# Performance work log

Measured on AMD Instinct MI355X. Metric: run time of the kernel, lower is better.

Reference implementation:

```python
import jax, jax.numpy as jnp
import numpy as np

B, T, D, H, OUT = 1024, 2048, 5, 64, 128


def _lstm_layer(x, Wih, Whh, bih, bhh):
    """PyTorch-convention LSTM layer. x: [B,T,Din]; gate order i,f,g,o."""
    b, t = x.shape[0], x.shape[1]
    h = Whh.shape[1]
    # Precompute input projections for all timesteps (the only big GEMM).
    xp = jnp.einsum('btd,gd->btg', x, Wih) + bih + bhh        # [B,T,4H]
    xp = jnp.swapaxes(xp, 0, 1)                               # [T,B,4H]

    def step(carry, xt):
        hprev, cprev = carry
        gates = xt + hprev @ Whh.T                            # [B,4H]
        i, f, g, o = jnp.split(gates, 4, axis=-1)
        i = jax.nn.sigmoid(i)
        f = jax.nn.sigmoid(f)
        g = jnp.tanh(g)
        o = jax.nn.sigmoid(o)
        c = f * cprev + i * g
        hnew = o * jnp.tanh(c)
        return (hnew, c), hnew

    h0 = jnp.zeros((b, h), x.dtype)
    (hT, cT), hs = jax.lax.scan(step, (h0, h0), xp)
    return jnp.swapaxes(hs, 0, 1), hT                         # [B,T,H], [B,H]


def setup_inputs() -> dict:
    key = jax.random.key(0)
    ks = jax.random.split(key, 11)
    s = 1.0 / np.sqrt(H)  # PyTorch LSTM init range

    def u(k, shape):
        return jax.random.uniform(k, shape, jnp.float32, -s, s)

    return {
        'x': jax.random.normal(ks[0], (B, T, D), jnp.float32),
        'W_ih0': u(ks[1], (4 * H, D)),
        'W_hh0': u(ks[2], (4 * H, H)),
        'b_ih0': u(ks[3], (4 * H,)),
        'b_hh0': u(ks[4], (4 * H,)),
        'W_ih1': u(ks[5], (4 * H, H)),
        'W_hh1': u(ks[6], (4 * H, H)),
        'b_ih1': u(ks[7], (4 * H,)),
        'b_hh1': u(ks[8], (4 * H,)),
        'W_fc': u(ks[9], (OUT, H)),
        'b_fc': u(ks[10], (OUT,)),
    }


def reference(x, W_ih0, W_hh0, b_ih0, b_hh0, W_ih1, W_hh1, b_ih1, b_hh1, W_fc, b_fc):
    # Layer 1 over raw 5-dim signal; inter-layer dropout is inactive at inference.
    y1, _ = _lstm_layer(x, W_ih0, W_hh0, b_ih0, b_hh0)
    # Layer 2; only its final hidden state hn[-1] is used downstream.
    _, h2 = _lstm_layer(y1, W_ih1, W_hh1, b_ih1, b_hh1)
    return jax.nn.relu(h2 @ W_fc.T + b_fc)                    # [B,128]
```

## Files before the change

### kernel.cpp

```cpp
#include <hip/hip_runtime.h>
#include <math.h>

#define BATCH 1024
#define TSEQ  2048
#define DIN   5
#define H     64
#define BT    4
#define SSTR  144
#define NOUT  128

typedef _Float16 f16x8 __attribute__((ext_vector_type(8)));
typedef float    f32x4 __attribute__((ext_vector_type(4)));

#if __has_builtin(__builtin_amdgcn_rcpf)
__device__ __forceinline__ float rcp_fast(float x) { return __builtin_amdgcn_rcpf(x); }
#else
__device__ __forceinline__ float rcp_fast(float x) { return 1.0f / x; }
#endif

#define LOG2E 1.44269504088896f
#define MFMA16(A, B, C) __builtin_amdgcn_mfma_f32_16x16x32_f16((A), (B), (C), 0, 0, 0)

__device__ __forceinline__ float sigm2(float s) {
    return rcp_fast(1.0f + __builtin_amdgcn_exp2f(-s));
}
__device__ __forceinline__ float tanh2(float s) {
    return fmaf(-2.0f, rcp_fast(__builtin_amdgcn_exp2f(s) + 1.0f), 1.0f);
}

__device__ __forceinline__ void sync_lgkm() {
    asm volatile("s_waitcnt lgkmcnt(0)" ::: "memory");
    __builtin_amdgcn_s_barrier();
    asm volatile("" ::: "memory");
}

__global__ __launch_bounds__(512)
void lstm_mfma(const float* __restrict__ x,
               const float* __restrict__ Wih0, const float* __restrict__ Whh0,
               const float* __restrict__ bih0, const float* __restrict__ bhh0,
               const float* __restrict__ Wih1, const float* __restrict__ Whh1,
               const float* __restrict__ bih1, const float* __restrict__ bhh1,
               const float* __restrict__ Wfc,  const float* __restrict__ bfc,
               float* __restrict__ out)
{
    __shared__ alignas(16) _Float16 S[2][BT * SSTR];
    __shared__ alignas(16) float    h2f[BT][H];

    const int tid  = threadIdx.x;
    const int w    = tid >> 6;
    const int lane = tid & 63;
    const int col  = lane & 15;
    const int q    = lane >> 4;
    const int ww   = w & 3;
    const int lay  = w >> 2;
    const int hu   = 16 * ww + col;
    const int b0   = blockIdx.x * BT;

    for (int j = tid; j < 2 * BT * SSTR; j += 512)
        ((_Float16*)S)[j] = (_Float16)0.0f;

    const float sgl[4] = {LOG2E, LOG2E, 2.0f * LOG2E, LOG2E};

    f16x8 Bf[4][4];
    f32x4 bC[4];
    float wx[4][DIN];
    float b1s[4];
    #pragma unroll
    for (int g = 0; g < 4; ++g) {
        const int   row = g * 64 + hu;
        const float sg  = sgl[g];
        if (lay) {
            const float* wa = Wih1 + row * H;
            const float* wb = Whh1 + row * H;
            #pragma unroll
            for (int j = 0; j < 8; ++j) {
                const int k = q * 8 + j;
                Bf[g][0][j] = (_Float16)(wa[k]      * sg);
                Bf[g][1][j] = (_Float16)(wa[32 + k] * sg);
                Bf[g][2][j] = (_Float16)(wb[k]      * sg);
                Bf[g][3][j] = (_Float16)(wb[32 + k] * sg);
            }
            const float bb = (bih1[row] + bhh1[row]) * sg;
            bC[g] = f32x4{bb, bb, bb, bb};
        } else {
            const float* wh = Whh0 + row * H;
            #pragma unroll
            for (int j = 0; j < 8; ++j) {
                const int k = q * 8 + j;
                Bf[g][0][j] = (_Float16)(wh[k]      * sg);
                Bf[g][1][j] = (_Float16)(wh[32 + k] * sg);
            }
            #pragma unroll
            for (int j = 0; j < DIN; ++j)
                wx[g][j] = Wih0[row * DIN + j] * sg;
            b1s[g] = (bih0[row] + bhh0[row]) * sg;
        }
    }

    const float* xq = x + (size_t)(b0 + q) * TSEQ * DIN;
    float x0 = 0.f, x1 = 0.f, x2 = 0.f, x3 = 0.f, x4 = 0.f;
    float dxs[4] = {0.f, 0.f, 0.f, 0.f};
    if (lay == 0) {
        float a0 = xq[0], a1 = xq[1], a2 = xq[2], a3 = xq[3], a4 = xq[4];
        #pragma unroll
        for (int g = 0; g < 4; ++g) {
            float s = fmaf(a0, wx[g][0], b1s[g]);
            s = fmaf(a1, wx[g][1], s);
            s = fmaf(a2, wx[g][2], s);
            s = fmaf(a3, wx[g][3], s);
            dxs[g] = fmaf(a4, wx[g][4], s);
        }
        x0 = xq[DIN + 0]; x1 = xq[DIN + 1]; x2 = xq[DIN + 2];
        x3 = xq[DIN + 3]; x4 = xq[DIN + 4];
        xq += 2 * DIN;
    }

    const int ab  = (col >> 2) * SSTR + q * 8;
    const int wb1 = q * SSTR + hu;
    const int wb2 = q * SSTR + 64 + hu;
    float cst = 0.0f, h2fin = 0.0f;

    __syncthreads();

    #pragma unroll 1
    for (int i = 0; i <= TSEQ; ++i) {
        const _Float16* rb   = S[(i + 1) & 1];
        _Float16*       wbuf = S[i & 1];

        if (lay == 0) {
            const bool ld2 = (i + 2 < TSEQ);
            float n0, n1, n2, n3, n4;
            if (ld2) { n0 = xq[0]; n1 = xq[1]; n2 = xq[2]; n3 = xq[3]; n4 = xq[4]; xq += DIN; }

            f16x8 a0 = *(const f16x8*)&rb[ab];
            f16x8 a1 = *(const f16x8*)&rb[ab + 32];

            f32x4 d[4];
            __builtin_amdgcn_s_setprio(1);
            #pragma unroll
            for (int g = 0; g < 4; ++g) {
                f32x4 c0 = {dxs[g], 0.f, 0.f, 0.f};
                d[g] = MFMA16(a0, Bf[g][0], c0);
                d[g] = MFMA16(a1, Bf[g][1], d[g]);
            }
            __builtin_amdgcn_s_setprio(0);

            if (i < TSEQ) {
                float iv = sigm2(d[0][0]);
                float fv = sigm2(d[1][0]);
                float gv = tanh2(d[2][0]);
                float ov = sigm2(d[3][0]);
                cst = fmaf(fv, cst, iv * gv);
                wbuf[wb1] = (_Float16)(ov * tanh2(2.0f * LOG2E * cst));
            }
            if (i + 1 < TSEQ) {
                #pragma unroll
                for (int g = 0; g < 4; ++g) {
                    float s = fmaf(x0, wx[g][0], b1s[g]);
                    s = fmaf(x1, wx[g][1], s);
                    s = fmaf(x2, wx[g][2], s);
                    s = fmaf(x3, wx[g][3], s);
                    dxs[g] = fmaf(x4, wx[g][4], s);
                }
            }
            if (ld2) { x0 = n0; x1 = n1; x2 = n2; x3 = n3; x4 = n4; }
        } else {
            f16x8 ay0 = *(const f16x8*)&rb[ab];
            f16x8 ay1 = *(const f16x8*)&rb[ab + 32];
            f16x8 ah0 = *(const f16x8*)&rb[ab + 64];
            f16x8 ah1 = *(const f16x8*)&rb[ab + 96];
            f32x4 e[4], f[4];
            const f32x4 z4 = {0.f, 0.f, 0.f, 0.f};
            __builtin_amdgcn_s_setprio(1);
            #pragma unroll
            for (int g = 0; g < 4; ++g) {
                e[g] = MFMA16(ay0, Bf[g][0], bC[g]);
                e[g] = MFMA16(ay1, Bf[g][1], e[g]);
                f[g] = MFMA16(ah0, Bf[g][2], z4);
                f[g] = MFMA16(ah1, Bf[g][3], f[g]);
            }
            __builtin_amdgcn_s_setprio(0);
            if (i > 0) {
                float p0 = e[0][0] + f[0][0];
                float p1 = e[1][0] + f[1][0];
                float p2 = e[2][0] + f[2][0];
                float p3 = e[3][0] + f[3][0];
                float iv = sigm2(p0);
                float fv = sigm2(p1);
                float gv = tanh2(p2);
                float ov = sigm2(p3);
                cst = fmaf(fv, cst, iv * gv);
                h2fin = ov * tanh2(2.0f * LOG2E * cst);
                wbuf[wb2] = (_Float16)h2fin;
            }
        }
        sync_lgkm();
    }

    if (lay) h2f[q][hu] = h2fin;
    __syncthreads();
    {
        const int e = tid >> 7;
        const int o = tid & (NOUT - 1);
        const float4* wr = (const float4*)(Wfc + o * H);
        const float*  hv = h2f[e];
        float s0 = 0.f, s1 = 0.f, s2 = 0.f, s3 = 0.f;
        #pragma unroll
        for (int k = 0; k < H / 4; ++k) {
            float4 wv = wr[k];
            s0 = fmaf(wv.x, hv[4 * k + 0], s0);
            s1 = fmaf(wv.y, hv[4 * k + 1], s1);
            s2 = fmaf(wv.z, hv[4 * k + 2], s2);
            s3 = fmaf(wv.w, hv[4 * k + 3], s3);
        }
        float acc = bfc[o] + (s0 + s1) + (s2 + s3);
        out[(size_t)(b0 + e) * NOUT + o] = fmaxf(acc, 0.0f);
    }
}

extern "C" void kernel_launch(void* const* d_in, const int* in_sizes, int n_in,
                              void* d_out, int out_size, void* d_ws, size_t ws_size,
                              hipStream_t stream) {
    const float* x    = (const float*)d_in[0];
    const float* Wih0 = (const float*)d_in[1];
    const float* Whh0 = (const float*)d_in[2];
    const float* bih0 = (const float*)d_in[3];
    const float* bhh0 = (const float*)d_in[4];
    const float* Wih1 = (const float*)d_in[5];
    const float* Whh1 = (const float*)d_in[6];
    const float* bih1 = (const float*)d_in[7];
    const float* bhh1 = (const float*)d_in[8];
    const float* Wfc  = (const float*)d_in[9];
    const float* bfc  = (const float*)d_in[10];
    float* out = (float*)d_out;

    lstm_mfma<<<dim3(BATCH / BT), dim3(512), 0, stream>>>(
        x, Wih0, Whh0, bih0, bhh0, Wih1, Whh1, bih1, bhh1, Wfc, bfc, out);
}
```

Baseline: 1.029 ms.

## Split LSTM layers into producer/consumer block pairs linked by a global ring buffer

Each batch tile now runs as two 256-thread blocks: one computes layer 0 and writes its hidden states into a per-pair ring buffer in global memory, and the other consumes them to run layer 1 and the final FC. Progress is tracked with atomic flags every CHK steps, and the consumer prefetches the next step's input. This decouples the two recurrences so layer 1 no longer waits on layer 0 every step and each block syncs fewer waves per barrier. In exchange it adds global-memory traffic, spin-waiting, and a dependence on both blocks of a pair being resident at once, which can deadlock if they are not co-scheduled.

```diff
diff --git a/kernel.cpp b/kernel.cpp
--- a/kernel.cpp
+++ b/kernel.cpp
@@ -8,6 +8,8 @@
 #define BT    4
 #define SSTR  144
 #define NOUT  128
+#define RING_D 128
+#define CHK   16
 
 typedef _Float16 f16x8 __attribute__((ext_vector_type(8)));
 typedef float    f32x4 __attribute__((ext_vector_type(4)));
@@ -34,14 +36,16 @@
     asm volatile("" ::: "memory");
 }
 
-__global__ __launch_bounds__(512)
-void lstm_mfma(const float* __restrict__ x,
+__global__ __launch_bounds__(256, 2)
+void lstm_pair(const float* __restrict__ x,
                const float* __restrict__ Wih0, const float* __restrict__ Whh0,
                const float* __restrict__ bih0, const float* __restrict__ bhh0,
                const float* __restrict__ Wih1, const float* __restrict__ Whh1,
                const float* __restrict__ bih1, const float* __restrict__ bhh1,
                const float* __restrict__ Wfc,  const float* __restrict__ bfc,
-               float* __restrict__ out)
+               float* __restrict__ out,
+               int* __restrict__ pflag, int* __restrict__ cflag,
+               _Float16* __restrict__ ring)
 {
     __shared__ alignas(16) _Float16 S[2][BT * SSTR];
     __shared__ alignas(16) float    h2f[BT][H];
@@ -51,38 +55,29 @@
     const int lane = tid & 63;
     const int col  = lane & 15;
     const int q    = lane >> 4;
-    const int ww   = w & 3;
-    const int lay  = w >> 2;
-    const int hu   = 16 * ww + col;
-    const int b0   = blockIdx.x * BT;
-
-    for (int j = tid; j < 2 * BT * SSTR; j += 512)
+    const int hu   = 16 * w + col;
+    const int p    = blockIdx.x >> 1;
+    const int role = blockIdx.x & 1;
+    const int b0   = p * BT;
+
+    _Float16* rp = ring + (size_t)p * (RING_D * BT * H);
+
+    for (int j = tid; j < 2 * BT * SSTR; j += 256)
         ((_Float16*)S)[j] = (_Float16)0.0f;
 
     const float sgl[4] = {LOG2E, LOG2E, 2.0f * LOG2E, LOG2E};
 
-    f16x8 Bf[4][4];
-    f32x4 bC[4];
-    float wx[4][DIN];
-    float b1s[4];
-    #pragma unroll
-    for (int g = 0; g < 4; ++g) {
-        const int   row = g * 64 + hu;
-        const float sg  = sgl[g];
-        if (lay) {
-            const float* wa = Wih1 + row * H;
-            const float* wb = Whh1 + row * H;
-            #pragma unroll
-            for (int j = 0; j < 8; ++j) {
-                const int k = q * 8 + j;
-                Bf[g][0][j] = (_Float16)(wa[k]      * sg);
-                Bf[g][1][j] = (_Float16)(wa[32 + k] * sg);
-                Bf[g][2][j] = (_Float16)(wb[k]      * sg);
-                Bf[g][3][j] = (_Float16)(wb[32 + k] * sg);
-            }
-            const float bb = (bih1[row] + bhh1[row]) * sg;
-            bC[g] = f32x4{bb, bb, bb, bb};
-        } else {
+    const int ab  = (col >> 2) * SSTR + q * 8;
+    const int wb1 = q * SSTR + hu;
+    const int wb2 = q * SSTR + 64 + hu;
+
+    if (role == 0) {
+        f16x8 Bf[4][2];
+        float wx[4][DIN], b1s[4];
+        #pragma unroll
+        for (int g = 0; g < 4; ++g) {
+            const int   row = g * 64 + hu;
+            const float sg  = sgl[g];
             const float* wh = Whh0 + row * H;
             #pragma unroll
             for (int j = 0; j < 8; ++j) {
@@ -95,43 +90,46 @@
                 wx[g][j] = Wih0[row * DIN + j] * sg;
             b1s[g] = (bih0[row] + bhh0[row]) * sg;
         }
-    }
-
-    const float* xq = x + (size_t)(b0 + q) * TSEQ * DIN;
-    float x0 = 0.f, x1 = 0.f, x2 = 0.f, x3 = 0.f, x4 = 0.f;
-    float dxs[4] = {0.f, 0.f, 0.f, 0.f};
-    if (lay == 0) {
-        float a0 = xq[0], a1 = xq[1], a2 = xq[2], a3 = xq[3], a4 = xq[4];
-        #pragma unroll
-        for (int g = 0; g < 4; ++g) {
-            float s = fmaf(a0, wx[g][0], b1s[g]);
-            s = fmaf(a1, wx[g][1], s);
-            s = fmaf(a2, wx[g][2], s);
-            s = fmaf(a3, wx[g][3], s);
-            dxs[g] = fmaf(a4, wx[g][4], s);
-        }
-        x0 = xq[DIN + 0]; x1 = xq[DIN + 1]; x2 = xq[DIN + 2];
-        x3 = xq[DIN + 3]; x4 = xq[DIN + 4];
-        xq += 2 * DIN;
-    }
-
-    const int ab  = (col >> 2) * SSTR + q * 8;
-    const int wb1 = q * SSTR + hu;
-    const int wb2 = q * SSTR + 64 + hu;
-    float cst = 0.0f, h2fin = 0.0f;
-
-    __syncthreads();
-
-    #pragma unroll 1
-    for (int i = 0; i <= TSEQ; ++i) {
-        const _Float16* rb   = S[(i + 1) & 1];
-        _Float16*       wbuf = S[i & 1];
-
-        if (lay == 0) {
-            const bool ld2 = (i + 2 < TSEQ);
+
+        const float* xq = x + (size_t)(b0 + q) * TSEQ * DIN;
+        float x0, x1, x2, x3, x4;
+        float dxs[4];
+        {
+            float a0 = xq[0], a1 = xq[1], a2 = xq[2], a3 = xq[3], a4 = xq[4];
+            #pragma unroll
+            for (int g = 0; g < 4; ++g) {
+                float s = fmaf(a0, wx[g][0], b1s[g]);
+                s = fmaf(a1, wx[g][1], s);
+                s = fmaf(a2, wx[g][2], s);
+                s = fmaf(a3, wx[g][3], s);
+                dxs[g] = fmaf(a4, wx[g][4], s);
+            }
+            x0 = xq[DIN + 0]; x1 = xq[DIN + 1]; x2 = xq[DIN + 2];
+            x3 = xq[DIN + 3]; x4 = xq[DIN + 4];
+            xq += 2 * DIN;
+        }
+
+        float cst = 0.0f;
+        int consf = 0;
+        __syncthreads();
+
+        #pragma unroll 1
+        for (int t = 0; t < TSEQ; ++t) {
+            if (t >= RING_D) {
+                const int need = t - RING_D + 1;
+                while (consf < need) {
+                    consf = __hip_atomic_load(cflag + p, __ATOMIC_RELAXED,
+                                              __HIP_MEMORY_SCOPE_AGENT);
+                    if (consf >= need) break;
+                    __builtin_amdgcn_s_sleep(8);
+                }
+            }
+
+            const bool ld2 = (t + 2 < TSEQ);
             float n0, n1, n2, n3, n4;
             if (ld2) { n0 = xq[0]; n1 = xq[1]; n2 = xq[2]; n3 = xq[3]; n4 = xq[4]; xq += DIN; }
 
+            const _Float16* rb = S[(t + 1) & 1];
             f16x8 a0 = *(const f16x8*)&rb[ab];
             f16x8 a1 = *(const f16x8*)&rb[ab + 32];
 
@@ -145,15 +143,14 @@
             }
             __builtin_amdgcn_s_setprio(0);
 
-            if (i < TSEQ) {
-                float iv = sigm2(d[0][0]);
-                float fv = sigm2(d[1][0]);
-                float gv = tanh2(d[2][0]);
-                float ov = sigm2(d[3][0]);
-                cst = fmaf(fv, cst, iv * gv);
-                wbuf[wb1] = (_Float16)(ov * tanh2(2.0f * LOG2E * cst));
-            }
-            if (i + 1 < TSEQ) {
+            float iv = sigm2(d[0][0]);
+            float fv = sigm2(d[1][0]);
+            float gv = tanh2(d[2][0]);
+            float ov = sigm2(d[3][0]);
+            cst = fmaf(fv, cst, iv * gv);
+            const float hval = ov * tanh2(2.0f * LOG2E * cst);
+
+            if (t + 1 < TSEQ) {
                 #pragma unroll
                 for (int g = 0; g < 4; ++g) {
                     float s = fmaf(x0, wx[g][0], b1s[g]);
@@ -164,57 +161,140 @@
                 }
             }
             if (ld2) { x0 = n0; x1 = n1; x2 = n2; x3 = n3; x4 = n4; }
-        } else {
-            f16x8 ay0 = *(const f16x8*)&rb[ab];
-            f16x8 ay1 = *(const f16x8*)&rb[ab + 32];
+
+            const _Float16 hv16 = (_Float16)hval;
+            S[t & 1][wb1] = hv16;
+            rp[((t & (RING_D - 1)) * BT + q) * H + hu] = hv16;
+
+            if ((t & (CHK - 1)) == CHK - 1) {
+                asm volatile("s_waitcnt vmcnt(0)" ::: "memory");
+                sync_lgkm();
+                if (tid == 0)
+                    __hip_atomic_store(pflag + p, t + 1, __ATOMIC_RELEASE,
+                                       __HIP_MEMORY_SCOPE_AGENT);
+            } else {
+                sync_lgkm();
+            }
+        }
+    } else {
+        f16x8 Bf[4][4];
+        f32x4 bC[4];
+        #pragma unroll
+        for (int g = 0; g < 4; ++g) {
+            const int   row = g * 64 + hu;
+            const float sg  = sgl[g];
+            const float* wa = Wih1 + row * H;
+            const float* wb = Whh1 + row * H;
+            #pragma unroll
+            for (int j = 0; j < 8; ++j) {
+                const int k = q * 8 + j;
+                Bf[g][0][j] = (_Float16)(wa[k]      * sg);
+                Bf[g][1][j] = (_Float16)(wa[32 + k] * sg);
+                Bf[g][2][j] = (_Float16)(wb[k]      * sg);
+                Bf[g][3][j] = (_Float16)(wb[32 + k] * sg);
+            }
+            const float bb = (bih1[row] + bhh1[row]) * sg;
+            bC[g] = f32x4{bb, bb, bb, bb};
+        }
+
+        float cst = 0.0f, h2fin = 0.0f;
+        int pf = 0;
+        const int yoff = (col >> 2) * H + q * 8;
+
+        __syncthreads();
+
+        while (pf < 1) {
+            pf = __hip_atomic_load(pflag + p, __ATOMIC_ACQUIRE, __HIP_MEMORY_SCOPE_AGENT);
+            if (pf >= 1) break;
+            __builtin_amdgcn_s_sleep(8);
+        }
+        f16x8 cy0 = *(const f16x8*)&rp[yoff];
+        f16x8 cy1 = *(const f16x8*)&rp[yoff + 32];
+
+        #pragma unroll 1
+        for (int t = 0; t < TSEQ; ++t) {
+            f16x8 ny0, ny1;
+            const bool pre = (t + 1 < TSEQ);
+            if (pre) {
+                if (pf < t + 2) {
+                    while (pf < t + 2) {
+                        pf = __hip_atomic_load(pflag + p, __ATOMIC_ACQUIRE,
+                                               __HIP_MEMORY_SCOPE_AGENT);
+                        if (pf >= t + 2) break;
+                        __builtin_amdgcn_s_sleep(8);
+                    }
+                }
+                const int so = ((t + 1) & (RING_D - 1)) * (BT * H);
+                ny0 = *(const f16x8*)&rp[so + yoff];
+                ny1 = *(const f16x8*)&rp[so + yoff + 32];
+            }
+
+            f32x4 e[4];
+            __builtin_amdgcn_s_setprio(1);
+            #pragma unroll
+            for (int g = 0; g < 4; ++g) {
+                e[g] = MFMA16(cy0, Bf[g][0], bC[g]);
+                e[g] = MFMA16(cy1, Bf[g][1], e[g]);
+            }
+            __builtin_amdgcn_s_setprio(0);
+
+            sync_lgkm();
+
+            if ((t & (CHK - 1)) == 0 && t > 0 && tid == 0)
+                __hip_atomic_store(cflag + p, t, __ATOMIC_RELAXED,
+                                   __HIP_MEMORY_SCOPE_AGENT);
+
+            const _Float16* rb = S[(t + 1) & 1];
             f16x8 ah0 = *(const f16x8*)&rb[ab + 64];
             f16x8 ah1 = *(const f16x8*)&rb[ab + 96];
-            f32x4 e[4], f[4];
+
+            f32x4 f[4];
             const f32x4 z4 = {0.f, 0.f, 0.f, 0.f};
             __builtin_amdgcn_s_setprio(1);
             #pragma unroll
             for (int g = 0; g < 4; ++g) {
-                e[g] = MFMA16(ay0, Bf[g][0], bC[g]);
-                e[g] = MFMA16(ay1, Bf[g][1], e[g]);
                 f[g] = MFMA16(ah0, Bf[g][2], z4);
                 f[g] = MFMA16(ah1, Bf[g][3], f[g]);
             }
             __builtin_amdgcn_s_setprio(0);
-            if (i > 0) {
-                float p0 = e[0][0] + f[0][0];
-                float p1 = e[1][0] + f[1][0];
-                float p2 = e[2][0] + f[2][0];
-                float p3 = e[3][0] + f[3][0];
-                float iv = sigm2(p0);
-                float fv = sigm2(p1);
-                float gv = tanh2(p2);
-                float ov = sigm2(p3);
-                cst = fmaf(fv, cst, iv * gv);
-                h2fin = ov * tanh2(2.0f * LOG2E * cst);
-                wbuf[wb2] = (_Float16)h2fin;
-            }
-        }
-        sync_lgkm();
-    }
-
-    if (lay) h2f[q][hu] = h2fin;
-    __syncthreads();
-    {
-        const int e = tid >> 7;
-        const int o = tid & (NOUT - 1);
-        const float4* wr = (const float4*)(Wfc + o * H);
-        const float*  hv = h2f[e];
-        float s0 = 0.f, s1 = 0.f, s2 = 0.f, s3 = 0.f;
-        #pragma unroll
-        for (int k = 0; k < H / 4; ++k) {
-            float4 wv = wr[k];
-            s0 = fmaf(wv.x, hv[4 * k + 0], s0);
-            s1 = fmaf(wv.y, hv[4 * k + 1], s1);
-            s2 = fmaf(wv.z, hv[4 * k + 2], s2);
-            s3 = fmaf(wv.w, hv[4 * k + 3], s3);
-        }
-        float acc = bfc[o] + (s0 + s1) + (s2 + s3);
-        out[(size_t)(b0 + e) * NOUT + o] = fmaxf(acc, 0.0f);
+
+            float p0 = e[0][0] + f[0][0];
+            float p1 = e[1][0] + f[1][0];
+            float p2 = e[2][0] + f[2][0];
+            float p3 = e[3][0] + f[3][0];
+            float iv = sigm2(p0);
+            float fv = sigm2(p1);
+            float gv = tanh2(p2);
+            float ov = sigm2(p3);
+            cst = fmaf(fv, cst, iv * gv);
+            h2fin = ov * tanh2(2.0f * LOG2E * cst);
+            S[t & 1][wb2] = (_Float16)h2fin;
+
+            if (pre) { cy0 = ny0; cy1 = ny1; }
+        }
+
+        h2f[q][hu] = h2fin;
+        __syncthreads();
+        {
+            const int o  = tid & (NOUT - 1);
+            const int eh = tid >> 7;
+            const float4* wr = (const float4*)(Wfc + o * H);
+            #pragma unroll
+            for (int e2 = eh; e2 < BT; e2 += 2) {
+                const float* hv = h2f[e2];
+                float s0 = 0.f, s1 = 0.f, s2 = 0.f, s3 = 0.f;
+                #pragma unroll
+                for (int k = 0; k < H / 4; ++k) {
+                    float4 wv = wr[k];
+                    s0 = fmaf(wv.x, hv[4 * k + 0], s0);
+                    s1 = fmaf(wv.y, hv[4 * k + 1], s1);
+                    s2 = fmaf(wv.z, hv[4 * k + 2], s2);
+                    s3 = fmaf(wv.w, hv[4 * k + 3], s3);
+                }
+                float acc = bfc[o] + (s0 + s1) + (s2 + s3);
+                out[(size_t)(b0 + e2) * NOUT + o] = fmaxf(acc, 0.0f);
+            }
+        }
     }
 }
 
@@ -234,6 +314,13 @@
     const float* bfc  = (const float*)d_in[10];
     float* out = (float*)d_out;
 
-    lstm_mfma<<<dim3(BATCH / BT), dim3(512), 0, stream>>>(
-        x, Wih0, Whh0, bih0, bhh0, Wih1, Whh1, bih1, bhh1, Wfc, bfc, out);
-}
+    int*      pflag = (int*)d_ws;
+    int*      cflag = (int*)d_ws + 256;
+    _Float16* ring  = (_Float16*)((char*)d_ws + 4096);
+
+    hipMemsetAsync(d_ws, 0, 2048, stream);
+
+    lstm_pair<<<dim3(2 * (BATCH / BT)), dim3(256), 0, stream>>>(
+        x, Wih0, Whh0, bih0, bhh0, Wih1, Whh1, bih1, bhh1, Wfc, bfc, out,
+        pflag, cflag, ring);
+}
```

New measurement: 2.617 ms. +154.4%, slower.
